# Kernel tuning notes

Measured on AMD Instinct MI355X. Metric: run time of the kernel, lower is better.

The kernel has to match this reference:

```python
import jax, jax.numpy as jnp
import numpy as np

B, T, C, DU, OUT = 16, 2048, 1024, 1024, 512
CIF_THRESHOLD = 1.0


def setup_inputs():
    key = jax.random.key(0)
    k0, k1, k2, k3, k4, k5 = jax.random.split(key, 6)
    encoder_out = jax.random.normal(k0, (B, T, C), dtype=jnp.float32)
    input_lengths = (T // 2 + jax.random.randint(k1, (B,), 0, T // 2)).astype(jnp.int32)
    target_lengths = (200 + jax.random.randint(k2, (B,), 0, 300)).astype(jnp.int32)
    s = 1.0 / np.sqrt(C)
    Wd = jax.random.uniform(k3, (DU, C), jnp.float32, -s, s)
    bd = jnp.zeros((DU,), jnp.float32)
    sp = 1.0 / np.sqrt(DU)
    Wp = jax.random.uniform(k4, (1, DU), jnp.float32, -sp, sp)
    bp = jnp.zeros((1,), jnp.float32)
    Wo = jax.random.uniform(k5, (OUT, C), jnp.float32, -s, s)
    return {"encoder_out": encoder_out, "input_lengths": input_lengths,
            "target_lengths": target_lengths, "Wd": Wd, "bd": bd,
            "Wp": Wp, "bp": bp, "Wo": Wo}


def _cif_forward(encoder_out, input_lengths, target_lengths, Wd, bd, Wp, bp, Wo):
    Bsz, Tlen, Cdim = encoder_out.shape
    pos = jnp.arange(Tlen)
    not_pad = (pos[None, :] < input_lengths[:, None]).astype(encoder_out.dtype)  # [B,T]

    # dense weight production: relu(x Wd^T + bd) -> sigmoid(. Wp^T + bp)
    h = jax.nn.relu(jnp.einsum('btc,dc->btd', encoder_out, Wd) + bd)
    weight = jax.nn.sigmoid(jnp.einsum('btd,od->bto', h, Wp)[..., 0] + bp[0])
    org_weight = weight * not_pad

    # training-time scaling so weights sum to target_lengths
    scale = target_lengths.astype(encoder_out.dtype) / (org_weight.sum(-1) + 1e-8)
    weight = org_weight * scale[:, None]

    padding_start_id = input_lengths  # = not_padding_mask.sum(-1)

    def step(carry, xs):
        acc_w, acc_s = carry                     # [B], [B,C]
        w, e, i = xs                             # [B], [B,C], scalar step idx
        fired = (acc_w + w) >= CIF_THRESHOLD     # [B]
        remained = 1.0 - acc_w
        new_w = jnp.where(fired, w - remained, w + acc_w)
        new_s = jnp.where(fired[:, None], (w - remained)[:, None] * e,
                          acc_s + w[:, None] * e)
        f_s = jnp.where(fired[:, None], acc_s + remained[:, None] * e, 0.0)
        f_s = jnp.where((i > padding_start_id)[:, None], 0.0, f_s)
        return (new_w, new_s), f_s

    init = (jnp.zeros((Bsz,), encoder_out.dtype),
            jnp.zeros((Bsz, Cdim), encoder_out.dtype))
    _, fired_states = jax.lax.scan(
        step, init,
        (weight.T, jnp.transpose(encoder_out, (1, 0, 2)), jnp.arange(Tlen)))
    fired_states = jnp.transpose(fired_states, (1, 0, 2))  # [B,T,C]

    fired_marks = jnp.abs(fired_states).sum(-1) != 0.0     # [B,T]
    # stable-compact fired frames to front; pad to T (upper bound of fired_max_length)
    order = jnp.argsort(jnp.logical_not(fired_marks).astype(jnp.int32), axis=1)
    n_fired = fired_marks.sum(-1)                           # [B]
    valid = pos[None, :] < n_fired[:, None]                 # [B,T]
    cif_outputs = jnp.take_along_axis(fired_states, order[:, :, None], axis=1)
    cif_outputs = cif_outputs * valid[:, :, None].astype(cif_outputs.dtype)

    idx = jnp.where(valid, order, 0).astype(jnp.int32)
    prev = jnp.concatenate([jnp.zeros((Bsz, 1), jnp.int32), idx[:, :-1]], axis=1)
    cif_durations = (idx - prev) * valid.astype(jnp.int32)

    base_mask = (pos[None, :] == 0).astype(jnp.int32)       # [1,0,0,...] fallback
    cif_out_padding_mask = jnp.where((n_fired > 0)[:, None],
                                     valid.astype(jnp.int32), base_mask)
    quantity_out = org_weight.sum(-1)                       # training branch
    cif_outputs = jnp.einsum('btc,oc->bto', cif_outputs, Wo)  # bias-free output proj
    return cif_outputs, cif_out_padding_mask, cif_durations, quantity_out


def reference(encoder_out, input_lengths, target_lengths, Wd, bd, Wp, bp, Wo):
    return _cif_forward(encoder_out, input_lengths, target_lengths,
                        Wd, bd, Wp, bp, Wo)
```

## Files before the change

kernel.cpp:

```cpp
#include <hip/hip_runtime.h>
#include <cstdint>
#include <cstddef>

#define BSZ 16
#define TLEN 2048
#define CDIM 1024
#define OUTDIM 512
#define MAXF 512

typedef _Float16 f16x8 __attribute__((ext_vector_type(8)));
typedef _Float16 f16x4 __attribute__((ext_vector_type(4)));
typedef float f32x16 __attribute__((ext_vector_type(16)));

__device__ __forceinline__ void gl_lds16(const void* g, void* l) {
    __builtin_amdgcn_global_load_lds(
        (const __attribute__((address_space(1))) void*)g,
        (__attribute__((address_space(3))) void*)l, 16, 0, 0);
}

struct h2pair { _Float16 h0, h1; };
__device__ __forceinline__ h2pair split2(float a) {
    h2pair o;
    o.h0 = (_Float16)a;
    float r = a - (float)o.h0;
    o.h1 = (_Float16)(r * 2048.0f);
    return o;
}

__global__ __launch_bounds__(128) void k0a_split_wd(
    const float* __restrict__ Wd, _Float16* __restrict__ B0,
    _Float16* __restrict__ B1)
{
    const int dut = blockIdx.x;
    const int ktl = blockIdx.y;
    const int r = threadIdx.x;
    const float* src = Wd + (size_t)(dut * 128 + r) * CDIM + ktl * 32;
    float v[32];
#pragma unroll
    for (int j = 0; j < 8; j++) *(float4*)&v[j * 4] = *(const float4*)(src + j * 4);
    const size_t tb = (size_t)(dut * 32 + ktl) * 4096;
#pragma unroll
    for (int c = 0; c < 4; c++) {
        f16x8 h0, h1;
#pragma unroll
        for (int j = 0; j < 8; j++) {
            h2pair s = split2(v[c * 8 + j]);
            h0[j] = s.h0;
            h1[j] = s.h1;
        }
        *(f16x8*)&B0[tb + (c * 128 + r) * 8] = h0;
        *(f16x8*)&B1[tb + (c * 128 + r) * 8] = h1;
    }
}

__global__ __launch_bounds__(256) void k0c_split_wo(
    const float* __restrict__ Wo, _Float16* __restrict__ W0,
    _Float16* __restrict__ W1)
{
    const int i = (blockIdx.x * 256 + threadIdx.x) * 4;
    float4 v = *(const float4*)(Wo + i);
    f16x4 h0, h1;
    h2pair s0 = split2(v.x); h0[0] = s0.h0; h1[0] = s0.h1;
    h2pair s1 = split2(v.y); h0[1] = s1.h0; h1[1] = s1.h1;
    h2pair s2 = split2(v.z); h0[2] = s2.h0; h1[2] = s2.h1;
    h2pair s3 = split2(v.w); h0[3] = s3.h0; h1[3] = s3.h1;
    *(f16x4*)&W0[i] = h0;
    *(f16x4*)&W1[i] = h1;
}

__global__ __launch_bounds__(256, 2) void k1_weight_gemm(
    const float* __restrict__ enc, const _Float16* __restrict__ BT0,
    const _Float16* __restrict__ BT1, const float* __restrict__ bd,
    const float* __restrict__ Wp, float* __restrict__ g)
{
    __shared__ __align__(16) _Float16 lds[16384];

    const int tid = threadIdx.x;
    const int lane = tid & 63;
    const int wv = tid >> 6;
    const int l5 = lane & 31;
    const int hi = lane >> 5;
    const int mtb = (wv & 1) * 64;
    const int ntb = (wv >> 1) * 64;

    const int bx = blockIdx.x;
    const int dut = bx & 7;
    const long row0 = (long)(bx >> 3) * 128;
    const int du0 = dut * 128;

    const int sr = tid >> 1;
    const int sh = tid & 1;
    const float* aptr = enc + (row0 + sr) * (long)CDIM + sh * 16;

    const _Float16* btile = ((wv >> 1) ? BT1 : BT0) + (size_t)dut * 32 * 4096;
    const int bh = wv & 1;
    _Float16* blds = &lds[8192 + (wv >> 1) * 4096 + bh * 2048];

    f32x16 acc[2][2], accc[2][2];
#pragma unroll
    for (int mt = 0; mt < 2; mt++)
#pragma unroll
        for (int nt = 0; nt < 2; nt++)
#pragma unroll
            for (int r = 0; r < 16; r++) { acc[mt][nt][r] = 0.f; accc[mt][nt][r] = 0.f; }

    float fa[16];
#pragma unroll
    for (int j = 0; j < 4; j++) *(float4*)&fa[j * 4] = *(const float4*)(aptr + j * 4);

    for (int kt = 0; kt < 32; ++kt) {
        f16x8 va0[2], va1[2];
#pragma unroll
        for (int c = 0; c < 2; c++)
#pragma unroll
            for (int j = 0; j < 8; j++) {
                h2pair s = split2(fa[c * 8 + j]);
                va0[c][j] = s.h0;
                va1[c][j] = s.h1;
            }

        __syncthreads();
#pragma unroll
        for (int c = 0; c < 2; c++) {
            *(f16x8*)&lds[((sh * 2 + c) * 128 + sr) * 8] = va0[c];
            *(f16x8*)&lds[4096 + ((sh * 2 + c) * 128 + sr) * 8] = va1[c];
        }
#pragma unroll
        for (int c = 0; c < 4; c++) {
            gl_lds16(btile + (size_t)kt * 4096 + (bh * 256 + c * 64 + lane) * 8,
                     blds + c * 512);
        }
        __syncthreads();

        if (kt < 31) {
#pragma unroll
            for (int j = 0; j < 4; j++)
                *(float4*)&fa[j * 4] = *(const float4*)(aptr + (kt + 1) * 32 + j * 4);
        }

#pragma unroll
        for (int ks = 0; ks < 2; ks++) {
            const int ch = ks * 2 + hi;
            f16x8 A0[2], A1[2], B0[2], B1[2];
#pragma unroll
            for (int mt = 0; mt < 2; mt++) {
                const int row = mtb + mt * 32 + l5;
                A0[mt] = *(const f16x8*)&lds[(ch * 128 + row) * 8];
                A1[mt] = *(const f16x8*)&lds[4096 + (ch * 128 + row) * 8];
            }
#pragma unroll
            for (int nt = 0; nt < 2; nt++) {
                const int row = ntb + nt * 32 + l5;
                B0[nt] = *(const f16x8*)&lds[8192 + (ch * 128 + row) * 8];
                B1[nt] = *(const f16x8*)&lds[12288 + (ch * 128 + row) * 8];
            }
#pragma unroll
            for (int mt = 0; mt < 2; mt++)
#pragma unroll
                for (int nt = 0; nt < 2; nt++) {
                    acc[mt][nt] = __builtin_amdgcn_mfma_f32_32x32x16_f16(
                        A0[mt], B0[nt], acc[mt][nt], 0, 0, 0);
                    accc[mt][nt] = __builtin_amdgcn_mfma_f32_32x32x16_f16(
                        A0[mt], B1[nt], accc[mt][nt], 0, 0, 0);
                    accc[mt][nt] = __builtin_amdgcn_mfma_f32_32x32x16_f16(
                        A1[mt], B0[nt], accc[mt][nt], 0, 0, 0);
                }
        }
    }

    float bdv[2], wpv[2];
#pragma unroll
    for (int nt = 0; nt < 2; nt++) {
        int n = du0 + ntb + nt * 32 + l5;
        bdv[nt] = bd[n];
        wpv[nt] = Wp[n];
    }
    float pm[2][16];
#pragma unroll
    for (int mt = 0; mt < 2; mt++)
#pragma unroll
        for (int r = 0; r < 16; r++) {
            float s = 0.f;
#pragma unroll
            for (int nt = 0; nt < 2; nt++) {
                float h = acc[mt][nt][r] + 4.8828125e-4f * accc[mt][nt][r] + bdv[nt];
                h = h > 0.f ? h : 0.f;
                s += wpv[nt] * h;
            }
            s += __shfl_xor(s, 1);
            s += __shfl_xor(s, 2);
            s += __shfl_xor(s, 4);
            s += __shfl_xor(s, 8);
            s += __shfl_xor(s, 16);
            pm[mt][r] = s;
        }
    float out = 0.f;
#pragma unroll
    for (int mt = 0; mt < 2; mt++)
#pragma unroll
        for (int r = 0; r < 16; r++)
            if (l5 == mt * 16 + r) out = pm[mt][r];
    const int mt_sel = l5 >> 4;
    const int r_sel = l5 & 15;
    const int row = mtb + mt_sel * 32 + (r_sel & 3) + 8 * (r_sel >> 2) + 4 * hi;
    atomicAdd(&g[row0 + row], out);
}

__global__ __launch_bounds__(256) void k2_scan(
    const float* __restrict__ g, const int* __restrict__ in_len,
    const int* __restrict__ tgt_len, const float* __restrict__ bp,
    float* __restrict__ c_a, float* __restrict__ c_b,
    int* __restrict__ fire_t, int* __restrict__ n_fired,
    float* __restrict__ out_mask, float* __restrict__ out_dur,
    float* __restrict__ out_qty)
{
    __shared__ float w[TLEN];
    __shared__ float ca[TLEN];
    __shared__ float cb[TLEN];
    __shared__ int fires[MAXF];
    __shared__ float ssum[256];
    __shared__ float s_scale;
    __shared__ int s_nf;

    const int b = blockIdx.x;
    const int tid = threadIdx.x;
    const int len = in_len[b];
    const float bpv = bp[0];

    float local = 0.f;
    for (int t = tid; t < TLEN; t += 256) {
        float gv = g[b * TLEN + t] + bpv;
        float s = 1.f / (1.f + expf(-gv));
        float ow = (t < len) ? s : 0.f;
        w[t] = ow;
        local += ow;
    }
    ssum[tid] = local;
    __syncthreads();
    for (int st = 128; st > 0; st >>= 1) {
        if (tid < st) ssum[tid] += ssum[tid + st];
        __syncthreads();
    }
    if (tid == 0) {
        float org_sum = ssum[0];
        out_qty[b] = org_sum;
        s_scale = (float)tgt_len[b] / (org_sum + 1e-8f);
    }
    __syncthreads();
    float scale = s_scale;
    for (int t = tid; t < TLEN; t += 256) w[t] *= scale;
    __syncthreads();

    if (tid == 0) {
        float accw = 0.f;
        int k = 0;
        for (int t = 0; t < len; t++) {
            float wt = w[t];
            float aw = accw + wt;
            bool f = (aw >= 1.0f);
            float rem = 1.0f - accw;
            float fb = wt - rem;
            ca[t] = f ? rem : wt;
            cb[t] = f ? fb : 0.f;
            fires[k & (MAXF - 1)] = t;
            k += f ? 1 : 0;
            accw = f ? fb : aw;
        }
        s_nf = (k < MAXF) ? k : MAXF;
        n_fired[b] = s_nf;
    }
    __syncthreads();

    for (int t = tid; t < len; t += 256) {
        c_a[b * TLEN + t] = ca[t];
        c_b[b * TLEN + t] = cb[t];
    }
    const int nf = s_nf;
    for (int j = tid; j < nf; j += 256) {
        int tj = fires[j];
        fire_t[b * MAXF + j] = tj;
        out_mask[b * TLEN + j] = 1.0f;
        int prev = (j == 0) ? 0 : fires[j - 1];
        out_dur[b * TLEN + j] = (float)(tj - prev);
    }
    if (tid == 0 && nf == 0) out_mask[b * TLEN] = 1.0f;
}

__global__ __launch_bounds__(256) void k3a_compact(
    const float* __restrict__ enc, const float* __restrict__ c_a,
    const float* __restrict__ c_b, const int* __restrict__ fire_t,
    const int* __restrict__ n_fired, _Float16* __restrict__ C0,
    _Float16* __restrict__ C1)
{
    const int b = blockIdx.y;
    const int k = blockIdx.x;
    const int tid = threadIdx.x;
    _Float16* d0 = C0 + ((size_t)b * MAXF + k) * CDIM + tid * 4;
    _Float16* d1 = C1 + ((size_t)b * MAXF + k) * CDIM + tid * 4;
    if (k >= n_fired[b]) {
        f16x4 z = {(_Float16)0.f, (_Float16)0.f, (_Float16)0.f, (_Float16)0.f};
        *(f16x4*)d0 = z;
        *(f16x4*)d1 = z;
        return;
    }
    const int tend = fire_t[b * MAXF + k];
    const int tprev = (k == 0) ? -1 : fire_t[b * MAXF + k - 1];
    float ax = 0.f, ay = 0.f, az = 0.f, aw = 0.f;
    const int tstart = (tprev < 0) ? 0 : tprev;
    for (int t = tstart; t <= tend; t++) {
        float coef = (t == tprev) ? c_b[b * TLEN + t] : c_a[b * TLEN + t];
        const float4 e = *(const float4*)(enc + ((size_t)b * TLEN + t) * CDIM + tid * 4);
        ax += coef * e.x;
        ay += coef * e.y;
        az += coef * e.z;
        aw += coef * e.w;
    }
    f16x4 h0, h1;
    h2pair s0 = split2(ax); h0[0] = s0.h0; h1[0] = s0.h1;
    h2pair s1 = split2(ay); h0[1] = s1.h0; h1[1] = s1.h1;
    h2pair s2 = split2(az); h0[2] = s2.h0; h1[2] = s2.h1;
    h2pair s3 = split2(aw); h0[3] = s3.h0; h1[3] = s3.h1;
    *(f16x4*)d0 = h0;
    *(f16x4*)d1 = h1;
}

__global__ __launch_bounds__(256, 2) void k3b_outproj(
    const _Float16* __restrict__ C0, const _Float16* __restrict__ C1,
    const _Float16* __restrict__ W0, const _Float16* __restrict__ W1,
    const int* __restrict__ n_fired, float* __restrict__ out0)
{
    __shared__ __align__(16) _Float16 lds[16384];

    const int b = blockIdx.z;
    const int nf = n_fired[b];
    const int j0 = blockIdx.x * 128;
    if (j0 >= nf) return;
    const int o0 = blockIdx.y * 128;
    const int tid = threadIdx.x;
    const int lane = tid & 63;
    const int wv = tid >> 6;
    const int l5 = lane & 31;
    const int hi = lane >> 5;
    const int mtb = (wv & 1) * 64;
    const int ntb = (wv >> 1) * 64;

    const int sr = tid >> 1;
    const int sh = tid & 1;
    const _Float16* a0p = C0 + ((size_t)b * MAXF + j0 + sr) * CDIM + sh * 16;
    const _Float16* a1p = C1 + ((size_t)b * MAXF + j0 + sr) * CDIM + sh * 16;
    const _Float16* b0p = W0 + (size_t)(o0 + sr) * CDIM + sh * 16;
    const _Float16* b1p = W1 + (size_t)(o0 + sr) * CDIM + sh * 16;

    f32x16 acc[2][2], accc[2][2];
#pragma unroll
    for (int mt = 0; mt < 2; mt++)
#pragma unroll
        for (int nt = 0; nt < 2; nt++)
#pragma unroll
            for (int r = 0; r < 16; r++) { acc[mt][nt][r] = 0.f; accc[mt][nt][r] = 0.f; }

    f16x8 xa0[2], xa1[2], xb0[2], xb1[2];
#pragma unroll
    for (int c = 0; c < 2; c++) {
        xa0[c] = *(const f16x8*)(a0p + c * 8);
        xa1[c] = *(const f16x8*)(a1p + c * 8);
        xb0[c] = *(const f16x8*)(b0p + c * 8);
        xb1[c] = *(const f16x8*)(b1p + c * 8);
    }

    for (int kt = 0; kt < 32; ++kt) {
        __syncthreads();
#pragma unroll
        for (int c = 0; c < 2; c++) {
            *(f16x8*)&lds[((sh * 2 + c) * 128 + sr) * 8] = xa0[c];
            *(f16x8*)&lds[4096 + ((sh * 2 + c) * 128 + sr) * 8] = xa1[c];
            *(f16x8*)&lds[8192 + ((sh * 2 + c) * 128 + sr) * 8] = xb0[c];
            *(f16x8*)&lds[12288 + ((sh * 2 + c) * 128 + sr) * 8] = xb1[c];
        }
        __syncthreads();
        if (kt < 31) {
            const int o = (kt + 1) * 32;
#pragma unroll
            for (int c = 0; c < 2; c++) {
                xa0[c] = *(const f16x8*)(a0p + o + c * 8);
                xa1[c] = *(const f16x8*)(a1p + o + c * 8);
                xb0[c] = *(const f16x8*)(b0p + o + c * 8);
                xb1[c] = *(const f16x8*)(b1p + o + c * 8);
            }
        }
#pragma unroll
        for (int ks = 0; ks < 2; ks++) {
            const int ch = ks * 2 + hi;
            f16x8 A0[2], A1[2], B0[2], B1[2];
#pragma unroll
            for (int mt = 0; mt < 2; mt++) {
                const int row = mtb + mt * 32 + l5;
                A0[mt] = *(const f16x8*)&lds[(ch * 128 + row) * 8];
                A1[mt] = *(const f16x8*)&lds[4096 + (ch * 128 + row) * 8];
            }
#pragma unroll
            for (int nt = 0; nt < 2; nt++) {
                const int row = ntb + nt * 32 + l5;
                B0[nt] = *(const f16x8*)&lds[8192 + (ch * 128 + row) * 8];
                B1[nt] = *(const f16x8*)&lds[12288 + (ch * 128 + row) * 8];
            }
#pragma unroll
            for (int mt = 0; mt < 2; mt++)
#pragma unroll
                for (int nt = 0; nt < 2; nt++) {
                    acc[mt][nt] = __builtin_amdgcn_mfma_f32_32x32x16_f16(
                        A0[mt], B0[nt], acc[mt][nt], 0, 0, 0);
                    accc[mt][nt] = __builtin_amdgcn_mfma_f32_32x32x16_f16(
                        A0[mt], B1[nt], accc[mt][nt], 0, 0, 0);
                    accc[mt][nt] = __builtin_amdgcn_mfma_f32_32x32x16_f16(
                        A1[mt], B0[nt], accc[mt][nt], 0, 0, 0);
                }
        }
    }

#pragma unroll
    for (int mt = 0; mt < 2; mt++)
#pragma unroll
        for (int nt = 0; nt < 2; nt++)
#pragma unroll
            for (int r = 0; r < 16; r++) {
                float val = acc[mt][nt][r] + 4.8828125e-4f * accc[mt][nt][r];
                int m = mtb + mt * 32 + (r & 3) + 8 * (r >> 2) + 4 * hi;
                int col = o0 + ntb + nt * 32 + l5;
                out0[((size_t)b * TLEN + j0 + m) * OUTDIM + col] = val;
            }
}

extern "C" void kernel_launch(void* const* d_in, const int* in_sizes, int n_in,
                              void* d_out, int out_size, void* d_ws, size_t ws_size,
                              hipStream_t stream)
{
    const float* enc = (const float*)d_in[0];
    const int* in_len = (const int*)d_in[1];
    const int* tgt_len = (const int*)d_in[2];
    const float* Wd = (const float*)d_in[3];
    const float* bd = (const float*)d_in[4];
    const float* Wp = (const float*)d_in[5];
    const float* bp = (const float*)d_in[6];
    const float* Wo = (const float*)d_in[7];

    char* ws = (char*)d_ws;
    float* g       = (float*)(ws + 0);
    float* c_a     = (float*)(ws + 131072);
    float* c_b     = (float*)(ws + 262144);
    int* fire_t    = (int*)(ws + 393216);
    int* n_fired   = (int*)(ws + 425984);
    _Float16* WdT0 = (_Float16*)(ws + 458752);
    _Float16* WdT1 = (_Float16*)(ws + 2555904);
    _Float16* Wo0  = (_Float16*)(ws + 4653056);
    _Float16* Wo1  = (_Float16*)(ws + 5701632);
    _Float16* C0   = (_Float16*)(ws + 6750208);
    _Float16* C1   = (_Float16*)(ws + 23527424);

    float* out0 = (float*)d_out;
    float* out_mask = out0 + (size_t)BSZ * TLEN * OUTDIM;
    float* out_dur = out_mask + (size_t)BSZ * TLEN;
    float* out_qty = out_dur + (size_t)BSZ * TLEN;

    (void)hipMemsetAsync(g, 0, 131072, stream);
    (void)hipMemsetAsync(d_out, 0, (size_t)out_size * 4, stream);

    k0a_split_wd<<<dim3(8, 32), 128, 0, stream>>>(Wd, WdT0, WdT1);
    k0c_split_wo<<<512, 256, 0, stream>>>(Wo, Wo0, Wo1);
    k1_weight_gemm<<<2048, 256, 0, stream>>>(enc, WdT0, WdT1, bd, Wp, g);
    k2_scan<<<BSZ, 256, 0, stream>>>(g, in_len, tgt_len, bp, c_a, c_b,
                                     fire_t, n_fired, out_mask, out_dur, out_qty);
    k3a_compact<<<dim3(MAXF, BSZ), 256, 0, stream>>>(enc, c_a, c_b, fire_t,
                                                     n_fired, C0, C1);
    k3b_outproj<<<dim3(4, 4, BSZ), 256, 0, stream>>>(C0, C1, Wo0, Wo1,
                                                     n_fired, out0);
}
```

Baseline: 644.9 us.

## Double-buffer LDS in weight GEMM, remap blocks per XCD, unroll CIF scan

After: 590.8 us. 8.4% less time.

```diff
diff --git a/kernel.cpp b/kernel.cpp
--- a/kernel.cpp
+++ b/kernel.cpp
@@ -73,7 +73,7 @@
     const _Float16* __restrict__ BT1, const float* __restrict__ bd,
     const float* __restrict__ Wp, float* __restrict__ g)
 {
-    __shared__ __align__(16) _Float16 lds[16384];
+    __shared__ __align__(16) _Float16 lds[32768];
 
     const int tid = threadIdx.x;
     const int lane = tid & 63;
@@ -84,17 +84,20 @@
     const int ntb = (wv >> 1) * 64;
 
     const int bx = blockIdx.x;
-    const int dut = bx & 7;
-    const long row0 = (long)(bx >> 3) * 128;
-    const int du0 = dut * 128;
+    const int xcd = bx & 7;
+    const int j = bx >> 3;
+    const int rg = xcd * 32 + (j >> 3);
+    const int du = j & 7;
+    const long row0 = (long)rg * 128;
+    const int du0 = du * 128;
 
     const int sr = tid >> 1;
     const int sh = tid & 1;
     const float* aptr = enc + (row0 + sr) * (long)CDIM + sh * 16;
 
-    const _Float16* btile = ((wv >> 1) ? BT1 : BT0) + (size_t)dut * 32 * 4096;
+    const _Float16* btile = ((wv >> 1) ? BT1 : BT0) + (size_t)du * 32 * 4096;
     const int bh = wv & 1;
-    _Float16* blds = &lds[8192 + (wv >> 1) * 4096 + bh * 2048];
+    const int bofs = 8192 + (wv >> 1) * 4096 + bh * 2048;
 
     f32x16 acc[2][2], accc[2][2];
 #pragma unroll
@@ -105,37 +108,64 @@
             for (int r = 0; r < 16; r++) { acc[mt][nt][r] = 0.f; accc[mt][nt][r] = 0.f; }
 
     float fa[16];
-#pragma unroll
-    for (int j = 0; j < 4; j++) *(float4*)&fa[j * 4] = *(const float4*)(aptr + j * 4);
-
-    for (int kt = 0; kt < 32; ++kt) {
+
+#pragma unroll
+    for (int jj = 0; jj < 4; jj++)
+        *(float4*)&fa[jj * 4] = *(const float4*)(aptr + jj * 4);
+    {
         f16x8 va0[2], va1[2];
 #pragma unroll
         for (int c = 0; c < 2; c++)
 #pragma unroll
-            for (int j = 0; j < 8; j++) {
-                h2pair s = split2(fa[c * 8 + j]);
-                va0[c][j] = s.h0;
-                va1[c][j] = s.h1;
-            }
-
-        __syncthreads();
+            for (int jj = 0; jj < 8; jj++) {
+                h2pair s = split2(fa[c * 8 + jj]);
+                va0[c][jj] = s.h0;
+                va1[c][jj] = s.h1;
+            }
 #pragma unroll
         for (int c = 0; c < 2; c++) {
             *(f16x8*)&lds[((sh * 2 + c) * 128 + sr) * 8] = va0[c];
             *(f16x8*)&lds[4096 + ((sh * 2 + c) * 128 + sr) * 8] = va1[c];
         }
 #pragma unroll
-        for (int c = 0; c < 4; c++) {
-            gl_lds16(btile + (size_t)kt * 4096 + (bh * 256 + c * 64 + lane) * 8,
-                     blds + c * 512);
-        }
+        for (int c = 0; c < 4; c++)
+            gl_lds16(btile + (bh * 256 + c * 64 + lane) * 8,
+                     &lds[bofs + c * 512]);
+    }
+#pragma unroll
+    for (int jj = 0; jj < 4; jj++)
+        *(float4*)&fa[jj * 4] = *(const float4*)(aptr + 32 + jj * 4);
+
+    for (int kt = 0; kt < 32; ++kt) {
+        const int cur = (kt & 1) * 16384;
+        const int nxt = ((kt & 1) ^ 1) * 16384;
+
         __syncthreads();
 
         if (kt < 31) {
 #pragma unroll
-            for (int j = 0; j < 4; j++)
-                *(float4*)&fa[j * 4] = *(const float4*)(aptr + (kt + 1) * 32 + j * 4);
+            for (int c = 0; c < 4; c++)
+                gl_lds16(btile + (size_t)(kt + 1) * 4096 + (bh * 256 + c * 64 + lane) * 8,
+                         &lds[nxt + bofs + c * 512]);
+            f16x8 va0[2], va1[2];
+#pragma unroll
+            for (int c = 0; c < 2; c++)
+#pragma unroll
+                for (int jj = 0; jj < 8; jj++) {
+                    h2pair s = split2(fa[c * 8 + jj]);
+                    va0[c][jj] = s.h0;
+                    va1[c][jj] = s.h1;
+                }
+#pragma unroll
+            for (int c = 0; c < 2; c++) {
+                *(f16x8*)&lds[nxt + ((sh * 2 + c) * 128 + sr) * 8] = va0[c];
+                *(f16x8*)&lds[nxt + 4096 + ((sh * 2 + c) * 128 + sr) * 8] = va1[c];
+            }
+            if (kt < 30) {
+#pragma unroll
+                for (int jj = 0; jj < 4; jj++)
+                    *(float4*)&fa[jj * 4] = *(const float4*)(aptr + (kt + 2) * 32 + jj * 4);
+            }
         }
 
 #pragma unroll
@@ -145,14 +175,14 @@
 #pragma unroll
             for (int mt = 0; mt < 2; mt++) {
                 const int row = mtb + mt * 32 + l5;
-                A0[mt] = *(const f16x8*)&lds[(ch * 128 + row) * 8];
-                A1[mt] = *(const f16x8*)&lds[4096 + (ch * 128 + row) * 8];
+                A0[mt] = *(const f16x8*)&lds[cur + (ch * 128 + row) * 8];
+                A1[mt] = *(const f16x8*)&lds[cur + 4096 + (ch * 128 + row) * 8];
             }
 #pragma unroll
             for (int nt = 0; nt < 2; nt++) {
                 const int row = ntb + nt * 32 + l5;
-                B0[nt] = *(const f16x8*)&lds[8192 + (ch * 128 + row) * 8];
-                B1[nt] = *(const f16x8*)&lds[12288 + (ch * 128 + row) * 8];
+                B0[nt] = *(const f16x8*)&lds[cur + 8192 + (ch * 128 + row) * 8];
+                B1[nt] = *(const f16x8*)&lds[cur + 12288 + (ch * 128 + row) * 8];
             }
 #pragma unroll
             for (int mt = 0; mt < 2; mt++)
@@ -254,7 +284,26 @@
     if (tid == 0) {
         float accw = 0.f;
         int k = 0;
-        for (int t = 0; t < len; t++) {
+        int t = 0;
+        for (; t + 8 <= len; t += 8) {
+            float4 wa = *(const float4*)&w[t];
+            float4 wb4 = *(const float4*)&w[t + 4];
+            float wv8[8] = {wa.x, wa.y, wa.z, wa.w, wb4.x, wb4.y, wb4.z, wb4.w};
+#pragma unroll
+            for (int u = 0; u < 8; u++) {
+                float wt = wv8[u];
+                float aw = accw + wt;
+                bool f = (aw >= 1.0f);
+                float rem = 1.0f - accw;
+                float fb = wt - rem;
+                ca[t + u] = f ? rem : wt;
+                cb[t + u] = f ? fb : 0.f;
+                fires[k & (MAXF - 1)] = t + u;
+                k += f ? 1 : 0;
+                accw = f ? fb : aw;
+            }
+        }
+        for (; t < len; t++) {
             float wt = w[t];
             float aw = accw + wt;
             bool f = (aw >= 1.0f);
@@ -276,12 +325,12 @@
         c_b[b * TLEN + t] = cb[t];
     }
     const int nf = s_nf;
-    for (int j = tid; j < nf; j += 256) {
-        int tj = fires[j];
-        fire_t[b * MAXF + j] = tj;
-        out_mask[b * TLEN + j] = 1.0f;
-        int prev = (j == 0) ? 0 : fires[j - 1];
-        out_dur[b * TLEN + j] = (float)(tj - prev);
+    for (int jj = tid; jj < nf; jj += 256) {
+        int tj = fires[jj];
+        fire_t[b * MAXF + jj] = tj;
+        out_mask[b * TLEN + jj] = 1.0f;
+        int prev = (jj == 0) ? 0 : fires[jj - 1];
+        out_dur[b * TLEN + jj] = (float)(tj - prev);
     }
     if (tid == 0 && nf == 0) out_mask[b * TLEN] = 1.0f;
 }
```
